# Kernel tuning notes

Measured on AMD Instinct MI355X. Metric: run time of the kernel, lower is better.

## Reference

```python
import jax, jax.numpy as jnp
import numpy as np

H = 16      # num_heads
DH = 64     # dim_heads


def rotate_half(x):
    # '... (j d) -> ... j d', j=2; unbind -> (x1, x2); cat(-x2, x1)
    x1, x2 = jnp.split(x, 2, axis=-1)
    return jnp.concatenate([-x2, x1], axis=-1)


def apply_rope(t, freqs):
    # t: [b, h, s, d], freqs: [s, d] (rot_dim == d, so no unrotated tail)
    return t * jnp.cos(freqs) + rotate_half(t) * jnp.sin(freqs)


def setup_inputs() -> dict:
    key = jax.random.key(0)
    k1, k2, k3, k4 = jax.random.split(key, 4)
    B, S, D = 2, 2048, 1024
    x = jax.random.normal(k1, (B, S, D), dtype=jnp.float32)
    w_qkv = jax.random.normal(k2, (D, 3 * D), dtype=jnp.float32) * (D ** -0.5)
    w_out = jax.random.normal(k3, (D, D), dtype=jnp.float32) * (D ** -0.5)
    freqs = jax.random.normal(k4, (S, DH), dtype=jnp.float32)
    return {"x": x, "w_qkv": w_qkv, "w_out": w_out, "freqs": freqs}


def reference(x, w_qkv, w_out, freqs):
    B, S, D = x.shape
    qkv = x @ w_qkv                                   # [B, S, 3D]
    q, k, v = jnp.split(qkv, 3, axis=-1)
    def to_heads(t):
        return t.reshape(B, S, H, DH).transpose(0, 2, 1, 3)  # [B, H, S, DH]
    q, k, v = map(to_heads, (q, k, v))
    # rotary (computed in float32, which is already the working dtype)
    q = apply_rope(q, freqs)
    k = apply_rope(k, freqs)
    # causal SDPA, scale = 1/sqrt(dh)
    scale = DH ** -0.5
    scores = jnp.einsum('bhqd,bhkd->bhqk', q, k) * scale
    causal_mask = jnp.tril(jnp.ones((S, S), dtype=bool))
    scores = jnp.where(causal_mask, scores, jnp.finfo(scores.dtype).min)
    attn = jax.nn.softmax(scores, axis=-1)
    out = jnp.einsum('bhqk,bhkd->bhqd', attn, v)      # [B, H, S, DH]
    out = out.transpose(0, 2, 1, 3).reshape(B, S, D)  # 'b h n d -> b n (h d)'
    return out @ w_out
```

## Files before the change

kernel.cpp:

```cpp
#include <hip/hip_runtime.h>


typedef __bf16 bf16x8 __attribute__((ext_vector_type(8)));
typedef float f32x4 __attribute__((ext_vector_type(4)));

__device__ __forceinline__ unsigned short f2b(float f) {
  unsigned int u = __builtin_bit_cast(unsigned int, f);
  unsigned int lsb = (u >> 16) & 1u;
  u += 0x7fffu + lsb;
  return (unsigned short)(u >> 16);
}
__device__ __forceinline__ float b2f(unsigned short h) {
  unsigned int u = ((unsigned int)h) << 16;
  return __builtin_bit_cast(float, u);
}
__device__ __forceinline__ unsigned int pk2(float a, float b) {
  return (unsigned int)f2b(a) | ((unsigned int)f2b(b) << 16);
}
__device__ __forceinline__ unsigned int cvtpk(float lo, float hi) {
  unsigned int r;
  asm("v_cvt_pk_bf16_f32 %0, %1, %2" : "=v"(r) : "v"(lo), "v"(hi));
  return r;
}
__device__ __forceinline__ void gload16(const void* g, void* l) {
  __builtin_amdgcn_global_load_lds(
      (const __attribute__((address_space(1))) unsigned int*)g,
      (__attribute__((address_space(3))) unsigned int*)l, 16, 0, 0);
}

__global__ __launch_bounds__(256) void prologue_kernel(
    const float* __restrict__ x, unsigned short* __restrict__ xb,
    const float* __restrict__ freqs, float* __restrict__ cosT,
    float* __restrict__ sinT, const float* __restrict__ w_qkv,
    unsigned short* __restrict__ wqT, const float* __restrict__ w_out,
    unsigned short* __restrict__ woT) {
  __shared__ float tile[32][33];
  const int blk = blockIdx.x, tid = threadIdx.x;

  if (blk < 4096) {
    int i = (blk * 256 + tid) * 4;
    float4 v = *(const float4*)&x[i];
    ushort4 o;
    o.x = f2b(v.x); o.y = f2b(v.y); o.z = f2b(v.z); o.w = f2b(v.w);
    *(ushort4*)&xb[i] = o;
    return;
  }
  if (blk < 4608) {
    int i = (blk - 4096) * 256 + tid;
    float f = freqs[i];
    cosT[i] = cosf(f);
    sinT[i] = sinf(f);
    return;
  }
  const float* src;
  unsigned short* dst;
  int K, N, bx, by;
  if (blk < 7680) {
    src = w_qkv; dst = wqT; K = 1024; N = 3072;
    const int t = blk - 4608;
    bx = t % 96; by = t / 96;
  } else {
    src = w_out; dst = woT; K = 1024; N = 1024;
    const int t = blk - 7680;
    bx = t % 32; by = t / 32;
  }
  const int n0 = bx * 32, k0 = by * 32;
  const int c = tid & 31, r4 = tid >> 5;
#pragma unroll
  for (int p = 0; p < 4; ++p) {
    int r = r4 + p * 8;
    tile[r][c] = src[(size_t)(k0 + r) * N + n0 + c];
  }
  __syncthreads();
#pragma unroll
  for (int p = 0; p < 4; ++p) {
    int r = r4 + p * 8;
    dst[(size_t)(n0 + r) * K + k0 + c] = f2b(tile[c][r]);
  }
}

__global__ __launch_bounds__(256, 2) void gemm_fused(
    const unsigned short* __restrict__ A, const unsigned short* __restrict__ BT,
    unsigned short* __restrict__ Qb, unsigned short* __restrict__ Kbp,
    unsigned short* __restrict__ Vtg, const float* __restrict__ cosT,
    const float* __restrict__ sinT) {
  extern __shared__ unsigned short L[];
  const int K = 1024;
  const int tid = threadIdx.x, lane = tid & 63, w = tid >> 6;
  const int wr = w >> 1, wc = w & 1;
  const int fr = lane & 15, oct = lane >> 4;

  const int m0 = blockIdx.y * 128, n0 = blockIdx.x * 192;

  const int sr = tid >> 2;
  const int scol = ((tid & 3) ^ ((tid >> 3) & 3)) * 8;
  const size_t aR0 = (size_t)(m0 + sr) * K + scol;
  const size_t aR1 = (size_t)(m0 + 64 + sr) * K + scol;
  const size_t bR0 = (size_t)(n0 + sr) * K + scol;
  const size_t bR1 = (size_t)(n0 + 64 + sr) * K + scol;
  const size_t bR2 = (size_t)(n0 + 128 + sr) * K + scol;

  f32x4 acc[4][6] = {};
  const int T = K >> 5;

  for (int pt = 0; pt < 3; ++pt) {
    unsigned short* Ln = &L[pt * 10240];
    const size_t gk = (size_t)pt * 32;
    gload16(&A[aR0 + gk], &Ln[tid * 8]);
    gload16(&A[aR1 + gk], &Ln[2048 + tid * 8]);
    gload16(&BT[bR0 + gk], &Ln[4096 + tid * 8]);
    gload16(&BT[bR1 + gk], &Ln[6144 + tid * 8]);
    gload16(&BT[bR2 + gk], &Ln[8192 + tid * 8]);
  }

  for (int t = 0; t < T; ++t) {
    if (t + 3 <= T) {
      asm volatile("s_waitcnt vmcnt(10)" ::: "memory");
    } else if (t + 2 == T) {
      asm volatile("s_waitcnt vmcnt(5)" ::: "memory");
    } else {
      asm volatile("s_waitcnt vmcnt(0)" ::: "memory");
    }
    __builtin_amdgcn_sched_barrier(0);
    __builtin_amdgcn_s_barrier();
    __builtin_amdgcn_sched_barrier(0);

    const unsigned short* Lb = &L[(t & 3) * 10240];
    unsigned short* Ln = &L[((t + 3) & 3) * 10240];
    const size_t gk = (size_t)(t + 3) * 32;
    const bool doStage = (t + 3 < T);

    bf16x8 af[4], bf[6];
#pragma unroll
    for (int i = 0; i < 4; ++i) {
      const int ra = wr * 64 + i * 16 + fr;
      af[i] = __builtin_bit_cast(
          bf16x8, *(const uint4*)&Lb[ra * 32 + ((oct ^ ((ra >> 1) & 3)) * 8)]);
    }
#pragma unroll
    for (int j = 0; j < 3; ++j) {
      const int rb = j * 32 + wc * 16 + fr;
      bf[j] = __builtin_bit_cast(
          bf16x8,
          *(const uint4*)&Lb[4096 + rb * 32 + ((oct ^ ((rb >> 1) & 3)) * 8)]);
    }
    if (doStage) {
      gload16(&A[aR0 + gk], &Ln[tid * 8]);
      gload16(&A[aR1 + gk], &Ln[2048 + tid * 8]);
      gload16(&BT[bR0 + gk], &Ln[4096 + tid * 8]);
    }
    __builtin_amdgcn_s_setprio(1);
#pragma unroll
    for (int i = 0; i < 4; ++i)
#pragma unroll
      for (int j = 0; j < 3; ++j)
        acc[i][j] = __builtin_amdgcn_mfma_f32_16x16x32_bf16(af[i], bf[j], acc[i][j], 0, 0, 0);
    __builtin_amdgcn_s_setprio(0);

#pragma unroll
    for (int j = 3; j < 6; ++j) {
      const int rb = j * 32 + wc * 16 + fr;
      bf[j] = __builtin_bit_cast(
          bf16x8,
          *(const uint4*)&Lb[4096 + rb * 32 + ((oct ^ ((rb >> 1) & 3)) * 8)]);
    }
    if (doStage) {
      gload16(&BT[bR1 + gk], &Ln[6144 + tid * 8]);
      gload16(&BT[bR2 + gk], &Ln[8192 + tid * 8]);
    }
    __builtin_amdgcn_s_setprio(1);
#pragma unroll
    for (int i = 0; i < 4; ++i)
#pragma unroll
      for (int j = 3; j < 6; ++j)
        acc[i][j] = __builtin_amdgcn_mfma_f32_16x16x32_bf16(af[i], bf[j], acc[i][j], 0, 0, 0);
    __builtin_amdgcn_s_setprio(0);
  }

  const float QSCALE = 0.125f * 1.44269504f;
  unsigned short* vtile = L + wr * (64 * 66);
#pragma unroll
  for (int jp = 0; jp < 3; ++jp) {
    const int gbase = n0 + jp * 64;
    const int part = gbase >> 10;
    const int hh = (gbase & 1023) >> 6;
    const int dlo = wc * 16 + fr;
    if (part < 2) {
      unsigned short* dst = (part == 0) ? Qb : Kbp;
      const float scale = (part == 0) ? QSCALE : 1.0f;
#pragma unroll
      for (int i = 0; i < 4; ++i) {
#pragma unroll
        for (int r = 0; r < 4; ++r) {
          const int m = m0 + wr * 64 + i * 16 + oct * 4 + r;
          const int bb = m >> 11, s = m & 2047;
          const float lo = acc[i][2 * jp][r], hi = acc[i][2 * jp + 1][r];
          const float cl = cosT[s * 64 + dlo], sl = sinT[s * 64 + dlo];
          const float ch = cosT[s * 64 + 32 + dlo], sh = sinT[s * 64 + 32 + dlo];
          const size_t ob = ((size_t)(bb * 16 + hh) * 2048 + s) * 64;
          dst[ob + dlo] = f2b((lo * cl - hi * sl) * scale);
          dst[ob + 32 + dlo] = f2b((hi * ch + lo * sh) * scale);
        }
      }
    } else {
      __syncthreads();
#pragma unroll
      for (int i = 0; i < 4; ++i)
#pragma unroll
        for (int r = 0; r < 4; ++r) {
          const int s64 = i * 16 + oct * 4 + r;
          vtile[s64 * 66 + dlo] = f2b(acc[i][2 * jp][r]);
          vtile[s64 * 66 + 32 + dlo] = f2b(acc[i][2 * jp + 1][r]);
        }
      __syncthreads();
      const int wrt = tid >> 7, t128 = tid & 127;
      const int d = t128 >> 1, q2h = t128 & 1;
      const unsigned short* tt = L + wrt * (64 * 66);
      const int mtile = m0 + wrt * 64;
      const int bb = mtile >> 11, sb = (mtile & 2047) >> 6;
      const size_t vb = (((size_t)(bb * 16 + hh) * 32 + sb) * 64 + d) * 64;
#pragma unroll
      for (int q2 = 0; q2 < 2; ++q2) {
        const int qq = q2h * 2 + q2;
#pragma unroll
        for (int g = 0; g < 4; ++g) {
          ushort4 u;
          u.x = tt[(qq * 16 + g * 4 + 0) * 66 + d];
          u.y = tt[(qq * 16 + g * 4 + 1) * 66 + d];
          u.z = tt[(qq * 16 + g * 4 + 2) * 66 + d];
          u.w = tt[(qq * 16 + g * 4 + 3) * 66 + d];
          *(ushort4*)&Vtg[vb + (qq >> 1) * 32 + g * 8 + (qq & 1) * 4] = u;
        }
      }
    }
  }
}

__global__ __launch_bounds__(256, 2) void gemm2_ring(const unsigned short* __restrict__ A,
                                                     const unsigned short* __restrict__ BT,
                                                     float* __restrict__ C,
                                                     int M, int N, int K) {
  extern __shared__ unsigned short L[];
  const int tid = threadIdx.x, lane = tid & 63, w = tid >> 6;
  const int wr = w >> 1, wc = w & 1;
  const int fr = lane & 15, oct = lane >> 4;
  const int m0 = blockIdx.y * 128, n0 = blockIdx.x * 64;

  const int sr = tid >> 2;
  const int scol = ((tid & 3) ^ ((tid >> 3) & 3)) * 8;
  const size_t aR0 = (size_t)(m0 + sr) * K + scol;
  const size_t aR1 = (size_t)(m0 + 64 + sr) * K + scol;
  const size_t bR0 = (size_t)(n0 + sr) * K + scol;

  f32x4 acc[4][2] = {};
  const int T = K >> 5;

  for (int pt = 0; pt < 3; ++pt) {
    unsigned short* Ln = &L[pt * 6144];
    const size_t gk = (size_t)pt * 32;
    gload16(&A[aR0 + gk], &Ln[tid * 8]);
    gload16(&A[aR1 + gk], &Ln[2048 + tid * 8]);
    gload16(&BT[bR0 + gk], &Ln[4096 + tid * 8]);
  }

  for (int t = 0; t < T; ++t) {
    if (t + 3 <= T) {
      asm volatile("s_waitcnt vmcnt(6)" ::: "memory");
    } else if (t + 2 == T) {
      asm volatile("s_waitcnt vmcnt(3)" ::: "memory");
    } else {
      asm volatile("s_waitcnt vmcnt(0)" ::: "memory");
    }
    __builtin_amdgcn_sched_barrier(0);
    __builtin_amdgcn_s_barrier();
    __builtin_amdgcn_sched_barrier(0);

    const unsigned short* Lb = &L[(t & 3) * 6144];
    unsigned short* Ln = &L[((t + 3) & 3) * 6144];
    const size_t gk = (size_t)(t + 3) * 32;
    const bool doStage = (t + 3 < T);

    bf16x8 af[4], bq[2];
#pragma unroll
    for (int i = 0; i < 4; ++i) {
      const int ra = wr * 64 + i * 16 + fr;
      af[i] = __builtin_bit_cast(
          bf16x8, *(const uint4*)&Lb[ra * 32 + ((oct ^ ((ra >> 1) & 3)) * 8)]);
    }
#pragma unroll
    for (int j = 0; j < 2; ++j) {
      const int rb = wc * 32 + j * 16 + fr;
      bq[j] = __builtin_bit_cast(
          bf16x8,
          *(const uint4*)&Lb[4096 + rb * 32 + ((oct ^ ((rb >> 1) & 3)) * 8)]);
    }
    if (doStage) {
      gload16(&A[aR0 + gk], &Ln[tid * 8]);
      gload16(&A[aR1 + gk], &Ln[2048 + tid * 8]);
      gload16(&BT[bR0 + gk], &Ln[4096 + tid * 8]);
    }
    __builtin_amdgcn_s_setprio(1);
#pragma unroll
    for (int i = 0; i < 4; ++i)
#pragma unroll
      for (int j = 0; j < 2; ++j)
        acc[i][j] = __builtin_amdgcn_mfma_f32_16x16x32_bf16(af[i], bq[j], acc[i][j], 0, 0, 0);
    __builtin_amdgcn_s_setprio(0);
  }

#pragma unroll
  for (int i = 0; i < 4; ++i)
#pragma unroll
    for (int j = 0; j < 2; ++j)
#pragma unroll
      for (int r = 0; r < 4; ++r)
        C[(size_t)(m0 + wr * 64 + i * 16 + oct * 4 + r) * N + n0 + wc * 32 +
          j * 16 + fr] = acc[i][j][r];
}

__global__ __launch_bounds__(512, 4) void attn_mfma(const unsigned short* __restrict__ Qb,
                                                    const unsigned short* __restrict__ Kb,
                                                    const unsigned short* __restrict__ Vtg,
                                                    unsigned short* __restrict__ attnb) {
  extern __shared__ unsigned short KV[];
  const int bid = blockIdx.x + 16 * (blockIdx.y + 16 * blockIdx.z);
  const int xcd = bid & 7, slot = bid >> 3;
  const int qt0 = slot & 15;
  const int gq = xcd + 8 * (slot >> 4);
  const int h = gq & 15, b = gq >> 4;
  const int qt1 = 31 - qt0;
  const int tid = threadIdx.x, lane = tid & 63, w = tid >> 6;
  const int fr = lane & 15, oct = lane >> 4;
  const int grp = w >> 2, wq = w & 3;
  const int nhA = 16 - qt0, nhB = 15 - qt0;

  const size_t bh = (size_t)(b * 16 + h);
  const unsigned short* Kbase = Kb + bh * 131072;
  const unsigned short* Vbase = Vtg + bh * 131072;

  const int qtP1 = grp ? qt1 : qt0;
  const unsigned short* Qp1 = Qb + (bh * 2048 + qtP1 * 64 + wq * 16 + fr) * 64;
  const bf16x8 qa0 = __builtin_bit_cast(bf16x8, *(const uint4*)(Qp1 + oct * 8));
  const bf16x8 qa1 = __builtin_bit_cast(bf16x8, *(const uint4*)(Qp1 + 32 + oct * 8));
  const unsigned short* Qp2 = Qb + (bh * 2048 + qt1 * 64 + wq * 16 + fr) * 64;
  const bf16x8 qb0 = __builtin_bit_cast(bf16x8, *(const uint4*)(Qp2 + oct * 8));
  const bf16x8 qb1 = __builtin_bit_cast(bf16x8, *(const uint4*)(Qp2 + 32 + oct * 8));

  float m_prev = -1e30f;
  f32x4 acc[4] = {};
  f32x4 accl = {};

  uint4 onesu;
  onesu.x = 0x3F803F80u; onesu.y = 0x3F803F80u;
  onesu.z = 0x3F803F80u; onesu.w = 0x3F803F80u;
  const bf16x8 onesf = __builtin_bit_cast(bf16x8, onesu);

  auto tile_step = [&](int buf, bf16x8 q0, bf16x8 q1, bool domask) {
    const unsigned short* Kbuf = &KV[buf * 4608];
    const unsigned short* Vbuf = &KV[(4 + buf) * 4608];
    f32x4 s4[4];
    __builtin_amdgcn_s_setprio(1);
#pragma unroll
    for (int t = 0; t < 4; ++t) {
      bf16x8 kf0 = __builtin_bit_cast(bf16x8, *(const uint4*)&Kbuf[(t * 16 + fr) * 72 + oct * 8]);
      bf16x8 kf1 = __builtin_bit_cast(bf16x8, *(const uint4*)&Kbuf[(t * 16 + fr) * 72 + 32 + oct * 8]);
      f32x4 s = {};
      s = __builtin_amdgcn_mfma_f32_16x16x32_bf16(kf0, q0, s, 0, 0, 0);
      s = __builtin_amdgcn_mfma_f32_16x16x32_bf16(kf1, q1, s, 0, 0, 0);
      s4[t] = s;
    }
    __builtin_amdgcn_s_setprio(0);
    if (domask) {
#pragma unroll
      for (int t = 0; t < 4; ++t)
#pragma unroll
        for (int r = 0; r < 4; ++r)
          if (t * 16 + oct * 4 + r > wq * 16 + fr) s4[t][r] = -1e30f;
    }

    float pm = -1e30f;
#pragma unroll
    for (int t = 0; t < 4; ++t)
#pragma unroll
      for (int r = 0; r < 4; ++r) pm = fmaxf(pm, s4[t][r]);
    const bool need = __any(pm - m_prev > 11.0f);
    if (need) {
      float pmf = fmaxf(pm, __shfl_xor(pm, 16));
      pmf = fmaxf(pmf, __shfl_xor(pmf, 32));
      float mnew = fmaxf(m_prev, pmf);
      float cf = __builtin_amdgcn_exp2f(m_prev - mnew);
      m_prev = mnew;
      float cfr[4];
#pragma unroll
      for (int r = 0; r < 4; ++r) cfr[r] = __shfl(cf, oct * 4 + r);
#pragma unroll
      for (int t2 = 0; t2 < 4; ++t2)
#pragma unroll
        for (int r = 0; r < 4; ++r) acc[t2][r] *= cfr[r];
#pragma unroll
      for (int r = 0; r < 4; ++r) accl[r] *= cfr[r];
    }
    const float mc = m_prev;
#pragma unroll
    for (int t = 0; t < 4; ++t)
#pragma unroll
      for (int r = 0; r < 4; ++r)
        s4[t][r] = __builtin_amdgcn_exp2f(s4[t][r] - mc);

    uint4 pw0, pw1;
    pw0.x = cvtpk(s4[0][0], s4[0][1]); pw0.y = cvtpk(s4[0][2], s4[0][3]);
    pw0.z = cvtpk(s4[1][0], s4[1][1]); pw0.w = cvtpk(s4[1][2], s4[1][3]);
    pw1.x = cvtpk(s4[2][0], s4[2][1]); pw1.y = cvtpk(s4[2][2], s4[2][3]);
    pw1.z = cvtpk(s4[3][0], s4[3][1]); pw1.w = cvtpk(s4[3][2], s4[3][3]);
    const bf16x8 pa0 = __builtin_bit_cast(bf16x8, pw0);
    const bf16x8 pa1 = __builtin_bit_cast(bf16x8, pw1);

    __builtin_amdgcn_s_setprio(1);
#pragma unroll
    for (int t2 = 0; t2 < 4; ++t2) {
      bf16x8 vf0 = __builtin_bit_cast(bf16x8, *(const uint4*)&Vbuf[(t2 * 16 + fr) * 72 + oct * 8]);
      bf16x8 vf1 = __builtin_bit_cast(bf16x8, *(const uint4*)&Vbuf[(t2 * 16 + fr) * 72 + 32 + oct * 8]);
      f32x4 a = acc[t2];
      a = __builtin_amdgcn_mfma_f32_16x16x32_bf16(pa0, vf0, a, 0, 0, 0);
      a = __builtin_amdgcn_mfma_f32_16x16x32_bf16(pa1, vf1, a, 0, 0, 0);
      acc[t2] = a;
    }
    {
      f32x4 a = accl;
      a = __builtin_amdgcn_mfma_f32_16x16x32_bf16(pa0, onesf, a, 0, 0, 0);
      a = __builtin_amdgcn_mfma_f32_16x16x32_bf16(pa1, onesf, a, 0, 0, 0);
      accl = a;
    }
    __builtin_amdgcn_s_setprio(0);
  };

  auto write_out = [&](int qtile) {
#pragma unroll
    for (int r = 0; r < 4; ++r) {
      float linv = 1.f / accl[r];
      size_t orow = (size_t)(b * 2048 + qtile * 64 + wq * 16 + oct * 4 + r);
#pragma unroll
      for (int t2 = 0; t2 < 4; ++t2)
        attnb[orow * 1024 + h * 64 + t2 * 16 + fr] = f2b(acc[t2][r] * linv);
    }
  };

  const int srow = tid >> 3, sc8 = (tid & 7) * 8;
  const unsigned short* kp1 = Kbase + srow * 64 + sc8;
  const unsigned short* vp1 = Vbase + srow * 64 + sc8;
  {
    uint4 kr = *(const uint4*)kp1;
    uint4 vr = *(const uint4*)vp1;
    *(uint4*)&KV[0 * 4608 + srow * 72 + sc8] = kr;
    *(uint4*)&KV[4 * 4608 + srow * 72 + sc8] = vr;
  }
  __syncthreads();

  for (int kb = 0; kb <= qt0; ++kb) {
    uint4 kr = *(const uint4*)(kp1 + (size_t)(kb + 1) * 4096);
    uint4 vr = *(const uint4*)(vp1 + (size_t)(kb + 1) * 4096);
    uint4 kr2, vr2;
    const bool extra = (kb == qt0) && (nhB > 0);
    if (extra) {
      kr2 = *(const uint4*)(kp1 + (size_t)17 * 4096);
      vr2 = *(const uint4*)(vp1 + (size_t)17 * 4096);
    }
    tile_step(kb & 1, qa0, qa1, kb == qtP1);
    const int nb = (kb + 1) & 1;
    *(uint4*)&KV[nb * 4608 + srow * 72 + sc8] = kr;
    *(uint4*)&KV[(4 + nb) * 4608 + srow * 72 + sc8] = vr;
    if (extra) {
      *(uint4*)&KV[2 * 4608 + srow * 72 + sc8] = kr2;
      *(uint4*)&KV[6 * 4608 + srow * 72 + sc8] = vr2;
    }
    __syncthreads();
  }

  if (grp == 0) {
    write_out(qt0);
    m_prev = -1e30f;
    f32x4 zz = {};
    accl = zz;
#pragma unroll
    for (int t2 = 0; t2 < 4; ++t2) acc[t2] = zz;
  }

  const int t2id = tid & 255;
  const int sk2 = t2id >> 2, sc2 = (t2id & 3) * 16;
  const int cnt = grp ? nhB : nhA;
  for (int i = 0; i < nhA; ++i) {
    const int kbm = grp ? (17 + i) : (qt0 + 1 + i);
    const int buf = grp ? (2 + (i & 1)) : (kbm & 1);
    uint4 k0, k1, v0, v1;
    const bool pf = (i + 1 < cnt);
    if (pf) {
      const unsigned short* ks = Kbase + (size_t)((kbm + 1) * 64 + sk2) * 64 + sc2;
      const unsigned short* vs = Vbase + (size_t)((kbm + 1) * 64 + sk2) * 64 + sc2;
      k0 = *(const uint4*)ks; k1 = *(const uint4*)(ks + 8);
      v0 = *(const uint4*)vs; v1 = *(const uint4*)(vs + 8);
    }
    if (i < cnt) tile_step(buf, qb0, qb1, kbm == qt1);
    if (pf) {
      const int nb = grp ? (2 + ((i + 1) & 1)) : ((kbm + 1) & 1);
      *(uint4*)&KV[nb * 4608 + sk2 * 72 + sc2] = k0;
      *(uint4*)&KV[nb * 4608 + sk2 * 72 + sc2 + 8] = k1;
      *(uint4*)&KV[(4 + nb) * 4608 + sk2 * 72 + sc2] = v0;
      *(uint4*)&KV[(4 + nb) * 4608 + sk2 * 72 + sc2 + 8] = v1;
    }
    __syncthreads();
  }

  float* MF = (float*)KV;
  if (grp == 1) {
#pragma unroll
    for (int t2 = 0; t2 < 4; ++t2)
#pragma unroll
      for (int r = 0; r < 4; ++r)
        MF[(wq * 16 + oct * 4 + r) * 68 + t2 * 16 + fr] = acc[t2][r];
    if (fr == 0) {
#pragma unroll
      for (int r = 0; r < 4; ++r) MF[4352 + wq * 16 + oct * 4 + r] = accl[r];
    }
    if (oct == 0) MF[4416 + wq * 16 + fr] = m_prev;
  }
  __syncthreads();
  if (grp == 0) {
    float mB = MF[4416 + wq * 16 + fr];
    float mS = fmaxf(m_prev, mB);
    float fA = __builtin_amdgcn_exp2f(m_prev - mS);
    float fB = __builtin_amdgcn_exp2f(mB - mS);
    float fAr[4], fBr[4];
#pragma unroll
    for (int r = 0; r < 4; ++r) {
      fAr[r] = __shfl(fA, oct * 4 + r);
      fBr[r] = __shfl(fB, oct * 4 + r);
    }
#pragma unroll
    for (int r = 0; r < 4; ++r)
      accl[r] = accl[r] * fAr[r] + MF[4352 + wq * 16 + oct * 4 + r] * fBr[r];
#pragma unroll
    for (int t2 = 0; t2 < 4; ++t2)
#pragma unroll
      for (int r = 0; r < 4; ++r)
        acc[t2][r] = acc[t2][r] * fAr[r] +
                     MF[(wq * 16 + oct * 4 + r) * 68 + t2 * 16 + fr] * fBr[r];
    write_out(qt1);
  }
}

extern "C" void kernel_launch(void* const* d_in, const int* in_sizes, int n_in,
                              void* d_out, int out_size, void* d_ws, size_t ws_size,
                              hipStream_t stream) {
  const float* x     = (const float*)d_in[0];
  const float* w_qkv = (const float*)d_in[1];
  const float* w_out = (const float*)d_in[2];
  const float* freqs = (const float*)d_in[3];
  float* out = (float*)d_out;

  char* ws = (char*)d_ws;
  unsigned short* Qb   = (unsigned short*)(ws + 25165824);
  unsigned short* Kb   = (unsigned short*)(ws + 33554432);
  unsigned short* Vtg  = (unsigned short*)(ws + 41943040);
  unsigned short* attnb= (unsigned short*)(ws + 50331648);
  unsigned short* wqT  = (unsigned short*)(ws + 58720256);
  unsigned short* woT  = (unsigned short*)(ws + 65011712);
  unsigned short* xb   = (unsigned short*)(ws + 67108864);
  float* cosT          = (float*)(ws + 75497472);
  float* sinT          = (float*)(ws + 76021760);

  (void)hipFuncSetAttribute((const void*)gemm_fused,
                            hipFuncAttributeMaxDynamicSharedMemorySize, 81920);
  (void)hipFuncSetAttribute((const void*)gemm2_ring,
                            hipFuncAttributeMaxDynamicSharedMemorySize, 49152);
  (void)hipFuncSetAttribute((const void*)attn_mfma,
                            hipFuncAttributeMaxDynamicSharedMemorySize, 73728);

  prologue_kernel<<<8704, 256, 0, stream>>>(x, xb, freqs, cosT, sinT, w_qkv,
                                            wqT, w_out, woT);
  gemm_fused<<<dim3(16, 32), 256, 81920, stream>>>(xb, wqT, Qb, Kb, Vtg, cosT,
                                                   sinT);
  attn_mfma<<<dim3(16, 16, 2), 512, 73728, stream>>>(Qb, Kb, Vtg, attnb);
  gemm2_ring<<<dim3(16, 32), 256, 49152, stream>>>(attnb, woT, out, 4096, 1024, 1024);
}
```

Measured before the change: 93.20 us.

## Shrink QKV GEMM tile to 128x128 with 3-stage ring and per-head epilogue

The fused QKV projection GEMM changes from 128x192 tiles with a 4-slot, 3-ahead LDS ring to 128x128 tiles with a 3-slot, 2-ahead ring. LDS drops from 80KB to 48KB and launch bounds rise to 3 blocks per CU, so the grid grows from 512 to 768 blocks. Each wave column now owns one full head, which simplifies the RoPE and V-transpose epilogue. The aim is better occupancy and CU fill, at the cost of less operand reuse per tile and a shallower prefetch pipeline.

Result: no change. 94.23 us (+1.1%).

```diff
diff --git a/kernel.cpp b/kernel.cpp
--- a/kernel.cpp
+++ b/kernel.cpp
@@ -79,7 +79,7 @@
   }
 }
 
-__global__ __launch_bounds__(256, 2) void gemm_fused(
+__global__ __launch_bounds__(256, 3) void gemm_fused(
     const unsigned short* __restrict__ A, const unsigned short* __restrict__ BT,
     unsigned short* __restrict__ Qb, unsigned short* __restrict__ Kbp,
     unsigned short* __restrict__ Vtg, const float* __restrict__ cosT,
@@ -90,7 +90,7 @@
   const int wr = w >> 1, wc = w & 1;
   const int fr = lane & 15, oct = lane >> 4;
 
-  const int m0 = blockIdx.y * 128, n0 = blockIdx.x * 192;
+  const int m0 = blockIdx.y * 128, n0 = blockIdx.x * 128;
 
   const int sr = tid >> 2;
   const int scol = ((tid & 3) ^ ((tid >> 3) & 3)) * 8;
@@ -98,26 +98,23 @@
   const size_t aR1 = (size_t)(m0 + 64 + sr) * K + scol;
   const size_t bR0 = (size_t)(n0 + sr) * K + scol;
   const size_t bR1 = (size_t)(n0 + 64 + sr) * K + scol;
-  const size_t bR2 = (size_t)(n0 + 128 + sr) * K + scol;
-
-  f32x4 acc[4][6] = {};
+
+  f32x4 acc[4][4] = {};
   const int T = K >> 5;
 
-  for (int pt = 0; pt < 3; ++pt) {
-    unsigned short* Ln = &L[pt * 10240];
+  for (int pt = 0; pt < 2; ++pt) {
+    unsigned short* Ln = &L[pt * 8192];
     const size_t gk = (size_t)pt * 32;
     gload16(&A[aR0 + gk], &Ln[tid * 8]);
     gload16(&A[aR1 + gk], &Ln[2048 + tid * 8]);
     gload16(&BT[bR0 + gk], &Ln[4096 + tid * 8]);
     gload16(&BT[bR1 + gk], &Ln[6144 + tid * 8]);
-    gload16(&BT[bR2 + gk], &Ln[8192 + tid * 8]);
-  }
-
+  }
+
+  int cs = 0;
   for (int t = 0; t < T; ++t) {
-    if (t + 3 <= T) {
-      asm volatile("s_waitcnt vmcnt(10)" ::: "memory");
-    } else if (t + 2 == T) {
-      asm volatile("s_waitcnt vmcnt(5)" ::: "memory");
+    if (t + 2 <= T) {
+      asm volatile("s_waitcnt vmcnt(4)" ::: "memory");
     } else {
       asm volatile("s_waitcnt vmcnt(0)" ::: "memory");
     }
@@ -125,12 +122,13 @@
     __builtin_amdgcn_s_barrier();
     __builtin_amdgcn_sched_barrier(0);
 
-    const unsigned short* Lb = &L[(t & 3) * 10240];
-    unsigned short* Ln = &L[((t + 3) & 3) * 10240];
-    const size_t gk = (size_t)(t + 3) * 32;
-    const bool doStage = (t + 3 < T);
-
-    bf16x8 af[4], bf[6];
+    const unsigned short* Lb = &L[cs * 8192];
+    const int sslot = (cs == 0) ? 2 : cs - 1;
+    unsigned short* Ln = &L[sslot * 8192];
+    const size_t gk = (size_t)(t + 2) * 32;
+    const bool doStage = (t + 2 < T);
+
+    bf16x8 af[4], bq[4];
 #pragma unroll
     for (int i = 0; i < 4; ++i) {
       const int ra = wr * 64 + i * 16 + fr;
@@ -138,9 +136,9 @@
           bf16x8, *(const uint4*)&Lb[ra * 32 + ((oct ^ ((ra >> 1) & 3)) * 8)]);
     }
 #pragma unroll
-    for (int j = 0; j < 3; ++j) {
-      const int rb = j * 32 + wc * 16 + fr;
-      bf[j] = __builtin_bit_cast(
+    for (int j = 0; j < 4; ++j) {
+      const int rb = wc * 64 + j * 16 + fr;
+      bq[j] = __builtin_bit_cast(
           bf16x8,
           *(const uint4*)&Lb[4096 + rb * 32 + ((oct ^ ((rb >> 1) & 3)) * 8)]);
     }
@@ -148,91 +146,72 @@
       gload16(&A[aR0 + gk], &Ln[tid * 8]);
       gload16(&A[aR1 + gk], &Ln[2048 + tid * 8]);
       gload16(&BT[bR0 + gk], &Ln[4096 + tid * 8]);
+      gload16(&BT[bR1 + gk], &Ln[6144 + tid * 8]);
     }
     __builtin_amdgcn_s_setprio(1);
 #pragma unroll
     for (int i = 0; i < 4; ++i)
 #pragma unroll
-      for (int j = 0; j < 3; ++j)
-        acc[i][j] = __builtin_amdgcn_mfma_f32_16x16x32_bf16(af[i], bf[j], acc[i][j], 0, 0, 0);
+      for (int j = 0; j < 4; ++j)
+        acc[i][j] = __builtin_amdgcn_mfma_f32_16x16x32_bf16(af[i], bq[j], acc[i][j], 0, 0, 0);
     __builtin_amdgcn_s_setprio(0);
 
-#pragma unroll
-    for (int j = 3; j < 6; ++j) {
-      const int rb = j * 32 + wc * 16 + fr;
-      bf[j] = __builtin_bit_cast(
-          bf16x8,
-          *(const uint4*)&Lb[4096 + rb * 32 + ((oct ^ ((rb >> 1) & 3)) * 8)]);
-    }
-    if (doStage) {
-      gload16(&BT[bR1 + gk], &Ln[6144 + tid * 8]);
-      gload16(&BT[bR2 + gk], &Ln[8192 + tid * 8]);
-    }
-    __builtin_amdgcn_s_setprio(1);
+    cs = (cs == 2) ? 0 : cs + 1;
+  }
+
+  const float QSCALE = 0.125f * 1.44269504f;
+  const int part = n0 >> 10;
+  const int hh = ((n0 & 1023) >> 6) + wc;
+  if (part < 2) {
+    unsigned short* dst = (part == 0) ? Qb : Kbp;
+    const float scale = (part == 0) ? QSCALE : 1.0f;
 #pragma unroll
     for (int i = 0; i < 4; ++i)
 #pragma unroll
-      for (int j = 3; j < 6; ++j)
-        acc[i][j] = __builtin_amdgcn_mfma_f32_16x16x32_bf16(af[i], bf[j], acc[i][j], 0, 0, 0);
-    __builtin_amdgcn_s_setprio(0);
-  }
-
-  const float QSCALE = 0.125f * 1.44269504f;
-  unsigned short* vtile = L + wr * (64 * 66);
-#pragma unroll
-  for (int jp = 0; jp < 3; ++jp) {
-    const int gbase = n0 + jp * 64;
-    const int part = gbase >> 10;
-    const int hh = (gbase & 1023) >> 6;
-    const int dlo = wc * 16 + fr;
-    if (part < 2) {
-      unsigned short* dst = (part == 0) ? Qb : Kbp;
-      const float scale = (part == 0) ? QSCALE : 1.0f;
-#pragma unroll
-      for (int i = 0; i < 4; ++i) {
-#pragma unroll
-        for (int r = 0; r < 4; ++r) {
-          const int m = m0 + wr * 64 + i * 16 + oct * 4 + r;
-          const int bb = m >> 11, s = m & 2047;
-          const float lo = acc[i][2 * jp][r], hi = acc[i][2 * jp + 1][r];
-          const float cl = cosT[s * 64 + dlo], sl = sinT[s * 64 + dlo];
-          const float ch = cosT[s * 64 + 32 + dlo], sh = sinT[s * 64 + 32 + dlo];
-          const size_t ob = ((size_t)(bb * 16 + hh) * 2048 + s) * 64;
-          dst[ob + dlo] = f2b((lo * cl - hi * sl) * scale);
-          dst[ob + 32 + dlo] = f2b((hi * ch + lo * sh) * scale);
+      for (int r = 0; r < 4; ++r) {
+        const int m = m0 + wr * 64 + i * 16 + oct * 4 + r;
+        const int bb = m >> 11, s = m & 2047;
+        const size_t ob = ((size_t)(bb * 16 + hh) * 2048 + s) * 64;
+#pragma unroll
+        for (int j = 0; j < 2; ++j) {
+          const int d = j * 16 + fr;
+          const float lo = acc[i][j][r], hi = acc[i][j + 2][r];
+          const float cl = cosT[s * 64 + d], sl = sinT[s * 64 + d];
+          const float ch = cosT[s * 64 + 32 + d], sh = sinT[s * 64 + 32 + d];
+          dst[ob + d] = f2b((lo * cl - hi * sl) * scale);
+          dst[ob + 32 + d] = f2b((hi * ch + lo * sh) * scale);
         }
       }
-    } else {
-      __syncthreads();
-#pragma unroll
-      for (int i = 0; i < 4; ++i)
-#pragma unroll
-        for (int r = 0; r < 4; ++r) {
-          const int s64 = i * 16 + oct * 4 + r;
-          vtile[s64 * 66 + dlo] = f2b(acc[i][2 * jp][r]);
-          vtile[s64 * 66 + 32 + dlo] = f2b(acc[i][2 * jp + 1][r]);
-        }
-      __syncthreads();
-      const int wrt = tid >> 7, t128 = tid & 127;
-      const int d = t128 >> 1, q2h = t128 & 1;
-      const unsigned short* tt = L + wrt * (64 * 66);
-      const int mtile = m0 + wrt * 64;
-      const int bb = mtile >> 11, sb = (mtile & 2047) >> 6;
-      const size_t vb = (((size_t)(bb * 16 + hh) * 32 + sb) * 64 + d) * 64;
-#pragma unroll
-      for (int q2 = 0; q2 < 2; ++q2) {
-        const int qq = q2h * 2 + q2;
-#pragma unroll
-        for (int g = 0; g < 4; ++g) {
-          ushort4 u;
-          u.x = tt[(qq * 16 + g * 4 + 0) * 66 + d];
-          u.y = tt[(qq * 16 + g * 4 + 1) * 66 + d];
-          u.z = tt[(qq * 16 + g * 4 + 2) * 66 + d];
-          u.w = tt[(qq * 16 + g * 4 + 3) * 66 + d];
-          *(ushort4*)&Vtg[vb + (qq >> 1) * 32 + g * 8 + (qq & 1) * 4] = u;
-        }
+  } else {
+    __syncthreads();
+    unsigned short* vt = L + (w)*4224;
+#pragma unroll
+    for (int i = 0; i < 4; ++i)
+#pragma unroll
+      for (int r = 0; r < 4; ++r) {
+        const int s64 = i * 16 + oct * 4 + r;
+#pragma unroll
+        for (int j = 0; j < 4; ++j) vt[s64 * 66 + j * 16 + fr] = f2b(acc[i][j][r]);
       }
-    }
+    __syncthreads();
+    const int tix = tid >> 6, d = tid & 63;
+    const int wrt = tix >> 1, wct = tix & 1;
+    const unsigned short* tt = L + tix * 4224;
+    const int mtile = m0 + wrt * 64;
+    const int bb = mtile >> 11, sb = (mtile & 2047) >> 6;
+    const int hv = ((n0 & 1023) >> 6) + wct;
+    const size_t vb = (((size_t)(bb * 16 + hv) * 32 + sb) * 64 + d) * 64;
+#pragma unroll
+    for (int qq = 0; qq < 4; ++qq)
+#pragma unroll
+      for (int g = 0; g < 4; ++g) {
+        ushort4 u;
+        u.x = tt[(qq * 16 + g * 4 + 0) * 66 + d];
+        u.y = tt[(qq * 16 + g * 4 + 1) * 66 + d];
+        u.z = tt[(qq * 16 + g * 4 + 2) * 66 + d];
+        u.w = tt[(qq * 16 + g * 4 + 3) * 66 + d];
+        *(ushort4*)&Vtg[vb + (qq >> 1) * 32 + g * 8 + (qq & 1) * 4] = u;
+      }
   }
 }
 
@@ -569,7 +548,7 @@
   float* sinT          = (float*)(ws + 76021760);
 
   (void)hipFuncSetAttribute((const void*)gemm_fused,
-                            hipFuncAttributeMaxDynamicSharedMemorySize, 81920);
+                            hipFuncAttributeMaxDynamicSharedMemorySize, 49152);
   (void)hipFuncSetAttribute((const void*)gemm2_ring,
                             hipFuncAttributeMaxDynamicSharedMemorySize, 49152);
   (void)hipFuncSetAttribute((const void*)attn_mfma,
@@ -577,7 +556,7 @@
 
   prologue_kernel<<<8704, 256, 0, stream>>>(x, xb, freqs, cosT, sinT, w_qkv,
                                             wqT, w_out, woT);
-  gemm_fused<<<dim3(16, 32), 256, 81920, stream>>>(xb, wqT, Qb, Kb, Vtg, cosT,
+  gemm_fused<<<dim3(24, 32), 256, 49152, stream>>>(xb, wqT, Qb, Kb, Vtg, cosT,
                                                    sinT);
   attn_mfma<<<dim3(16, 16, 2), 512, 73728, stream>>>(Qb, Kb, Vtg, attnb);
   gemm2_ring<<<dim3(16, 32), 256, 49152, stream>>>(attnb, woT, out, 4096, 1024, 1024);
```
